# Optimization experiments

Hardware: AMD Instinct MI355X
Metric: run time of the kernel (lower is better)

Reference implementation:

```python
import jax, jax.numpy as jnp
import numpy as np

BS = 2; D = 256; NH = 8; NL = 4; NP = 4; WS = 7; DFF = 1024
SHAPES = [(92, 92), (46, 46), (23, 23), (12, 12)]
LEN = sum(h * w for h, w in SHAPES)  # 11253
DH = D // NH


def _layer_norm(x, g, b):
    mu = jnp.mean(x, -1, keepdims=True)
    var = jnp.var(x, -1, keepdims=True)
    return (x - mu) * jax.lax.rsqrt(var + 1e-5) * g + b


def _bilinear(v_l, loc, H_, W_):
    # v_l: (N, nh, H_*W_, d); loc: (N, Lq, nh, P, 2) normalized in [0,1] (x, y)
    N, Lq, nh, P, _ = loc.shape
    x = loc[..., 0] * W_ - 0.5  # grid_sample align_corners=False convention
    y = loc[..., 1] * H_ - 0.5
    x0f = jnp.floor(x); y0f = jnp.floor(y)
    tx = (x - x0f).transpose(0, 2, 1, 3)  # (N, nh, Lq, P)
    ty = (y - y0f).transpose(0, 2, 1, 3)
    x0 = x0f.astype(jnp.int32).transpose(0, 2, 1, 3)
    y0 = y0f.astype(jnp.int32).transpose(0, 2, 1, 3)

    def g(yi, xi):
        valid = ((xi >= 0) & (xi < W_) & (yi >= 0) & (yi < H_)).astype(v_l.dtype)
        idx = (jnp.clip(yi, 0, H_ - 1) * W_ + jnp.clip(xi, 0, W_ - 1)).reshape(N, nh, Lq * P)
        out = jnp.take_along_axis(v_l, idx[..., None], axis=2).reshape(N, nh, Lq, P, -1)
        return out * valid[..., None]

    return (g(y0, x0) * ((1 - tx) * (1 - ty))[..., None]
            + g(y0, x0 + 1) * (tx * (1 - ty))[..., None]
            + g(y0 + 1, x0) * ((1 - tx) * ty)[..., None]
            + g(y0 + 1, x0 + 1) * (tx * ty)[..., None])


def setup_inputs() -> dict:
    key = jax.random.key(0)
    ks = jax.random.split(key, 20)
    s = 0.02
    inp = {}
    inp['src'] = jax.random.normal(ks[0], (BS, LEN, D), jnp.float32)
    inp['pos'] = jax.random.normal(ks[1], (BS, LEN, D), jnp.float32)
    inp['reference_points'] = jax.random.uniform(ks[2], (BS, LEN, NL, 2), jnp.float32)
    c = WS // 2
    ys, xs = jnp.meshgrid(jnp.arange(WS) - c, jnp.arange(WS) - c, indexing='ij')
    inp['window_grid'] = jnp.stack([xs, ys], -1).reshape(WS * WS, 2).astype(jnp.float32)
    for l, (h, w) in enumerate(SHAPES):
        inp[f'mask{l}'] = jax.random.normal(ks[3 + l], (BS, 1, h, w), jnp.float32)
    inp['spatial_shapes'] = jnp.array(SHAPES, jnp.int32)
    starts = np.cumsum([0] + [h * w for h, w in SHAPES])[:NL]
    inp['level_start_index'] = jnp.array(starts, jnp.int32)
    # parse_mask: Conv2d(1, n_heads, 1) per level -> per-head scale + bias
    inp['pm_w'] = jax.random.normal(ks[7], (NL, NH), jnp.float32) * s
    inp['pm_b'] = jax.random.normal(ks[8], (NL, NH), jnp.float32) * s
    inp['Wv'] = jax.random.normal(ks[9], (D, D), jnp.float32) * s
    inp['bv'] = jnp.zeros((D,), jnp.float32)
    inp['Wo'] = jax.random.normal(ks[10], (D, D), jnp.float32) * s
    inp['bo'] = jnp.zeros((D,), jnp.float32)
    inp['ln1_g'] = jnp.ones((D,), jnp.float32)
    inp['ln1_b'] = jnp.zeros((D,), jnp.float32)
    inp['W1'] = jax.random.normal(ks[11], (D, DFF), jnp.float32) * s
    inp['b1'] = jnp.zeros((DFF,), jnp.float32)
    inp['W2'] = jax.random.normal(ks[12], (DFF, D), jnp.float32) * s
    inp['b2'] = jnp.zeros((D,), jnp.float32)
    inp['ln2_g'] = jnp.ones((D,), jnp.float32)
    inp['ln2_b'] = jnp.zeros((D,), jnp.float32)
    return inp


def reference(src, pos, reference_points, window_grid, mask0, mask1, mask2, mask3,
              spatial_shapes, level_start_index, pm_w, pm_b, Wv, bv, Wo, bo,
              ln1_g, ln1_b, W1, b1, W2, b2, ln2_g, ln2_b):
    masks = [mask0, mask1, mask2, mask3]
    p = WS // 2
    offs, samp = [], []
    for l, (H_, W_) in enumerate(SHAPES):
        # 1x1 conv from 1 -> NH channels
        m = masks[l] * pm_w[l][None, :, None, None] + pm_b[l][None, :, None, None]  # (BS,NH,H,W)
        mp = jnp.pad(m, ((0, 0), (0, 0), (p, p), (p, p)))
        # unfold: (BS, NH, WS*WS, H*W), kernel positions row-major
        patches = jnp.stack([mp[:, :, i:i + H_, j:j + W_] for i in range(WS) for j in range(WS)], axis=2)
        patches = patches.reshape(BS, NH, WS * WS, H_ * W_).transpose(0, 1, 3, 2)  # (BS,NH,HW,WS^2)
        vals, idx = jax.lax.top_k(patches, NP)  # (BS,NH,HW,NP)
        off = window_grid[idx]  # (BS,NH,HW,NP,2)
        offs.append(off.transpose(0, 2, 1, 3, 4))   # (BS,HW,NH,NP,2)
        samp.append(vals.transpose(0, 2, 1, 3))     # (BS,HW,NH,NP)
    offsets = jnp.concatenate(offs, axis=1)       # (BS,LEN,NH,NP,2)
    pred_sampled = jnp.concatenate(samp, axis=1)  # (BS,LEN,NH,NP)

    # MSDeformAttn (encoder mode: external offsets + mask-derived attention logits)
    value = (src @ Wv + bv).reshape(BS, LEN, NH, DH)
    attn = jax.nn.softmax(
        jnp.broadcast_to(pred_sampled[:, :, :, None, :], (BS, LEN, NH, NL, NP)).reshape(BS, LEN, NH, NL * NP),
        axis=-1).reshape(BS, LEN, NH, NL, NP)
    norm = jnp.array([[w, h] for h, w in SHAPES], jnp.float32)  # (NL, 2) as (W, H)
    loc = reference_points[:, :, None, :, None, :] + offsets[:, :, :, None, :, :] / norm[None, None, None, :, None, :]

    out = jnp.zeros((BS, LEN, NH, DH), src.dtype)
    s0 = 0
    for l, (H_, W_) in enumerate(SHAPES):
        v_l = value[:, s0:s0 + H_ * W_].transpose(0, 2, 1, 3)  # (BS,NH,HW,DH)
        sampled = _bilinear(v_l, loc[:, :, :, l], H_, W_)       # (BS,NH,LEN,NP,DH)
        out = out + jnp.einsum('nhqpd,nqhp->nqhd', sampled, attn[:, :, :, l])
        s0 += H_ * W_
    attn_out = out.reshape(BS, LEN, D) @ Wo + bo

    x = _layer_norm(src + attn_out, ln1_g, ln1_b)
    x2 = jax.nn.relu(x @ W1 + b1) @ W2 + b2
    return _layer_norm(x + x2, ln2_g, ln2_b)
```

## Files before the change

kernel.cpp:

```cpp
#include <hip/hip_runtime.h>
#include <cstddef>
#include <cstdint>

#define LEN_T 11253
#define TOK   22506
#define NHEADS 8
#define DMODEL 256

#define SBAR() __builtin_amdgcn_sched_barrier(0)

typedef __attribute__((ext_vector_type(8))) short short8;
typedef __attribute__((ext_vector_type(4))) float f32x4;

__device__ __forceinline__ unsigned short f2bf(float f) {
  union { float f; unsigned u; } v; v.f = f;
  unsigned r = v.u + 0x7fffu + ((v.u >> 16) & 1u);
  return (unsigned short)(r >> 16);
}
__device__ __forceinline__ float bfhi2f(unsigned u) {
  union { unsigned u; float f; } v; v.u = u & 0xffff0000u; return v.f;
}
__device__ __forceinline__ float bflo2f(unsigned u) {
  union { unsigned u; float f; } v; v.u = u << 16; return v.f;
}
__device__ __forceinline__ float bf2f(unsigned short s) {
  union { unsigned u; float f; } v; v.u = (unsigned)s << 16; return v.f;
}
__device__ __forceinline__ void gld_lds16(const void* g, void* l) {
  __builtin_amdgcn_global_load_lds(
      (const __attribute__((address_space(1))) void*)g,
      (__attribute__((address_space(3))) void*)l, 16, 0, 0);
}

__device__ __forceinline__ void ins4(float v, int ji,
    float& t0, float& t1, float& t2, float& t3,
    int& i0, int& i1, int& i2, int& i3)
{
  bool a0 = v > t0, a1 = v > t1, a2 = v > t2, a3 = v > t3;
  t3 = a3 ? (a2 ? t2 : v) : t3;  i3 = a3 ? (a2 ? i2 : ji) : i3;
  t2 = a2 ? (a1 ? t1 : v) : t2;  i2 = a2 ? (a1 ? i1 : ji) : i2;
  t1 = a1 ? (a0 ? t0 : v) : t1;  i1 = a1 ? (a0 ? i0 : ji) : i1;
  t0 = a0 ? v : t0;              i0 = a0 ? ji : i0;
}

__global__ __launch_bounds__(256) void pre_kernel(
    const float* __restrict__ m0, const float* __restrict__ m1,
    const float* __restrict__ m2, const float* __restrict__ m3,
    const float* __restrict__ pm_w, const float* __restrict__ pm_b,
    const float* __restrict__ Wv, const float* __restrict__ Wo,
    const float* __restrict__ W1, const float* __restrict__ W2,
    unsigned short* __restrict__ Wv_g, unsigned short* __restrict__ Wo_g,
    unsigned short* __restrict__ W1_g, unsigned short* __restrict__ W2_g,
    unsigned* __restrict__ offp, float* __restrict__ attw)
{
  int blk = blockIdx.x;
  if (blk >= 704) {
    int cb = blk - 704;
    const float* W; unsigned short* Bg; int lgN, base;
    if (cb < 32)       { W = Wv; Bg = Wv_g; lgN = 8;  base = cb; }
    else if (cb < 64)  { W = Wo; Bg = Wo_g; lgN = 8;  base = cb - 32; }
    else if (cb < 192) { W = W1; Bg = W1_g; lgN = 10; base = cb - 64; }
    else               { W = W2; Bg = W2_g; lgN = 8;  base = cb - 192; }
    int idx = base * 256 + threadIdx.x;
    int s   = idx & 3;
    int n   = (idx >> 2) & ((1 << lgN) - 1);
    int kb  = idx >> (2 + lgN);
    int k0  = kb * 32 + ((s ^ ((n + (n >> 2)) & 3)) << 3);
    const float* wp = W + (size_t)k0 * (1 << lgN) + n;
    unsigned short e[8];
    #pragma unroll
    for (int j = 0; j < 8; ++j) e[j] = f2bf(wp[(size_t)j << lgN]);
    uint4 o;
    o.x = (unsigned)e[0] | ((unsigned)e[1] << 16);
    o.y = (unsigned)e[2] | ((unsigned)e[3] << 16);
    o.z = (unsigned)e[4] | ((unsigned)e[5] << 16);
    o.w = (unsigned)e[6] | ((unsigned)e[7] << 16);
    *(uint4*)(Bg + (size_t)idx * 8) = o;
    return;
  }
  int t = blk * 256 + threadIdx.x;
  if (t >= TOK * NHEADS) return;
  int h  = t & 7;
  int bq = t >> 3;
  int b  = bq / LEN_T;
  int q  = bq - b * LEN_T;
  int l, H_, W_;
  const float* mk;
  if (q < 8464)       { l = 0; H_ = 92; W_ = 92; mk = m0; }
  else if (q < 10580) { l = 1; H_ = 46; W_ = 46; mk = m1; }
  else if (q < 11109) { l = 2; H_ = 23; W_ = 23; mk = m2; }
  else                { l = 3; H_ = 12; W_ = 12; mk = m3; }
  int st = (l == 0) ? 0 : (l == 1) ? 8464 : (l == 2) ? 10580 : 11109;
  int pos = q - st;
  int rr = pos / W_;
  int cc = pos - rr * W_;
  float w  = pm_w[l * NHEADS + h];
  float bb = pm_b[l * NHEADS + h];
  const float* mp = mk + (size_t)b * H_ * W_;

  float t0=-1e30f,t1=-1e30f,t2=-1e30f,t3=-1e30f;
  int   i0=0,i1=0,i2=0,i3=0;
  for (int i = 0; i < 7; ++i) {
    int yy = rr + i - 3;
    #pragma unroll
    for (int j = 0; j < 7; ++j) {
      int xx = cc + j - 3;
      float v = 0.f;
      if (yy >= 0 && yy < H_ && xx >= 0 && xx < W_)
        v = mp[(size_t)yy * W_ + xx] * w + bb;
      ins4(v, j | (i << 4), t0, t1, t2, t3, i0, i1, i2, i3);
    }
  }
  float e1 = __expf(t1 - t0);
  float e2 = __expf(t2 - t0);
  float e3 = __expf(t3 - t0);
  float inv = 1.f / (4.f * (1.f + e1 + e2 + e3));
  float4 wout; wout.x = inv; wout.y = e1 * inv; wout.z = e2 * inv; wout.w = e3 * inv;
  *(float4*)(attw + (size_t)t * 4) = wout;
  offp[t] = (unsigned)i0 | ((unsigned)i1 << 8)
          | ((unsigned)i2 << 16) | ((unsigned)i3 << 24);
}

__global__ __launch_bounds__(256) void sample_kernel(
    const unsigned short* __restrict__ Vb, const float* __restrict__ refpts,
    const unsigned* __restrict__ offp, const float* __restrict__ attw,
    unsigned short* __restrict__ outp)
{
  __shared__ int4  sidx[4][128];
  __shared__ float4 swgt[4][128];
  const int wv   = threadIdx.x >> 6;
  const int lane = threadIdx.x & 63;
  const int bx = blockIdx.x & 7, by = blockIdx.x >> 3;
  const int nb = bx * 703 + min(bx, 3) + by;
  const int blk = nb * 4 + wv;
  const bool ok = blk < TOK;

  if (ok) {
    const int b = (blk >= LEN_T) ? 1 : 0;
    const float* rp = refpts + (size_t)blk * 8;
    #pragma unroll
    for (int e = 0; e < 2; ++e) {
      int t = lane * 2 + e;
      int h = t & 7, lp = t >> 3;
      int l = lp >> 2, p = lp & 3;
      unsigned pb = (offp[(size_t)blk * 8 + h] >> (8 * p)) & 0xffu;
      float ox = (float)(int)(pb & 15u) - 3.f;
      float oy = (float)(int)(pb >> 4)  - 3.f;
      float aw = attw[((size_t)blk * 8 + h) * 4 + p];
      int H_ = (l == 0) ? 92 : (l == 1) ? 46 : (l == 2) ? 23 : 12;
      int st = (l == 0) ? 0  : (l == 1) ? 8464 : (l == 2) ? 10580 : 11109;
      float xx = rp[2 * l]     * (float)H_ - 0.5f + ox;
      float yy = rp[2 * l + 1] * (float)H_ - 0.5f + oy;
      float x0f = floorf(xx), y0f = floorf(yy);
      float tx = xx - x0f, ty = yy - y0f;
      int x0 = (int)x0f, y0 = (int)y0f;
      int base = b * LEN_T + st;
      float wc[4] = {(1.f - tx) * (1.f - ty), tx * (1.f - ty),
                     (1.f - tx) * ty,         tx * ty};
      int4 idx; float4 wg;
      int xs[4] = {x0, x0 + 1, x0, x0 + 1};
      int ys[4] = {y0, y0, y0 + 1, y0 + 1};
      int   id[4]; float wgt[4];
      #pragma unroll
      for (int c = 0; c < 4; ++c) {
        int xi = xs[c], yi = ys[c];
        bool v_ = (xi >= 0) & (xi < H_) & (yi >= 0) & (yi < H_);
        id[c]  = base + min(max(yi, 0), H_ - 1) * H_ + min(max(xi, 0), H_ - 1);
        wgt[c] = v_ ? aw * wc[c] : 0.f;
      }
      idx.x = id[0]; idx.y = id[1]; idx.z = id[2]; idx.w = id[3];
      wg.x = wgt[0]; wg.y = wgt[1]; wg.z = wgt[2]; wg.w = wgt[3];
      sidx[wv][t] = idx;
      swgt[wv][t] = wg;
    }
  }
  __syncthreads();

  if (ok) {
    const int h = lane >> 3, dg = lane & 7;
    const unsigned short* vb = Vb + h * 32 + dg * 4;
    f32x4 acc = {0.f, 0.f, 0.f, 0.f};

    uint2  u[2][8];
    float4 wg[2][2];

    #pragma unroll
    for (int j = 0; j < 2; ++j) {
      int4 idx  = sidx[wv][j * 8 + h];
      wg[0][j]  = swgt[wv][j * 8 + h];
      u[0][j*4+0] = *(const uint2*)(vb + (size_t)idx.x * DMODEL);
      u[0][j*4+1] = *(const uint2*)(vb + (size_t)idx.y * DMODEL);
      u[0][j*4+2] = *(const uint2*)(vb + (size_t)idx.z * DMODEL);
      u[0][j*4+3] = *(const uint2*)(vb + (size_t)idx.w * DMODEL);
    }
    SBAR();
    #pragma unroll
    for (int bt = 0; bt < 8; ++bt) {
      const int cur = bt & 1, nxt = cur ^ 1;
      if (bt < 7) {
        #pragma unroll
        for (int j = 0; j < 2; ++j) {
          int lp = (bt + 1) * 2 + j;
          int4 idx   = sidx[wv][lp * 8 + h];
          wg[nxt][j] = swgt[wv][lp * 8 + h];
          u[nxt][j*4+0] = *(const uint2*)(vb + (size_t)idx.x * DMODEL);
          u[nxt][j*4+1] = *(const uint2*)(vb + (size_t)idx.y * DMODEL);
          u[nxt][j*4+2] = *(const uint2*)(vb + (size_t)idx.z * DMODEL);
          u[nxt][j*4+3] = *(const uint2*)(vb + (size_t)idx.w * DMODEL);
        }
      }
      SBAR();
      #pragma unroll
      for (int j = 0; j < 2; ++j) {
        const float4 w4 = wg[cur][j];
        const uint2 u0 = u[cur][j*4+0], u1 = u[cur][j*4+1];
        const uint2 u2 = u[cur][j*4+2], u3 = u[cur][j*4+3];
        acc.x += w4.x * bflo2f(u0.x) + w4.y * bflo2f(u1.x) + w4.z * bflo2f(u2.x) + w4.w * bflo2f(u3.x);
        acc.y += w4.x * bfhi2f(u0.x) + w4.y * bfhi2f(u1.x) + w4.z * bfhi2f(u2.x) + w4.w * bfhi2f(u3.x);
        acc.z += w4.x * bflo2f(u0.y) + w4.y * bflo2f(u1.y) + w4.z * bflo2f(u2.y) + w4.w * bflo2f(u3.y);
        acc.w += w4.x * bfhi2f(u0.y) + w4.y * bfhi2f(u1.y) + w4.z * bfhi2f(u2.y) + w4.w * bfhi2f(u3.y);
      }
    }
    uint2 o;
    o.x = (unsigned)f2bf(acc.x) | ((unsigned)f2bf(acc.y) << 16);
    o.y = (unsigned)f2bf(acc.z) | ((unsigned)f2bf(acc.w) << 16);
    *(uint2*)(outp + (size_t)blk * DMODEL + h * 32 + dg * 4) = o;
  }
}

template<int EPI, bool AF32, int KC>
__global__ __launch_bounds__(256, 3) void gemm_v7(
    const void* __restrict__ Aptr, const unsigned short* __restrict__ Bg,
    const float* __restrict__ bias, const float* __restrict__ res,
    const unsigned short* __restrict__ resb,
    const float* __restrict__ lng, const float* __restrict__ lnb,
    float* __restrict__ C, unsigned short* __restrict__ Cb,
    int M, int N)
{
  constexpr int K  = KC * 256;
  constexpr int NK = KC * 8;
  __shared__ short As[2][32 * 32]  __attribute__((aligned(16)));
  __shared__ short Bs[2][256 * 32] __attribute__((aligned(16)));
  __shared__ float2 lnred[32][4];
  const int tid = threadIdx.x, w = tid >> 6, lane = tid & 63;
  const int row0  = blockIdx.x * 32;
  const int ncol0 = blockIdx.y * 256;
  const int wn0   = ncol0 + w * 64;
  const int colq = lane & 15, quad = lane >> 4;

  f32x4 acc[2][4];
  #pragma unroll
  for (int i = 0; i < 2; ++i)
    #pragma unroll
    for (int j = 0; j < 4; ++j) acc[i][j] = (f32x4){0.f, 0.f, 0.f, 0.f};

  const int rA   = min(row0 + (tid >> 2), M - 1);
  const int ksw8 = (((tid & 3) ^ ((tid >> 3) & 3)) << 3);
  const float* Af = (const float*)Aptr;
  const short* Ab = (const short*)Aptr;

  auto stageA = [&](int kb, int nbuf) {
    if (tid < 128) {
      if constexpr (AF32) {
        const float* ap = Af + (size_t)rA * K + kb * 32 + ksw8;
        float4 f0 = *(const float4*)ap;
        float4 f1 = *(const float4*)(ap + 4);
        uint4 u;
        u.x = (unsigned)f2bf(f0.x) | ((unsigned)f2bf(f0.y) << 16);
        u.y = (unsigned)f2bf(f0.z) | ((unsigned)f2bf(f0.w) << 16);
        u.z = (unsigned)f2bf(f1.x) | ((unsigned)f2bf(f1.y) << 16);
        u.w = (unsigned)f2bf(f1.z) | ((unsigned)f2bf(f1.w) << 16);
        *(uint4*)(As[nbuf] + (size_t)tid * 8) = u;
      } else {
        gld_lds16(Ab + (size_t)rA * K + kb * 32 + ksw8,
                  As[nbuf] + (size_t)tid * 8);
      }
    }
  };
  auto stageB = [&](int kb, int nbuf) {
    const unsigned short* slab = Bg + ((size_t)kb * N + ncol0) * 32;
    #pragma unroll
    for (int j = 0; j < 4; ++j)
      gld_lds16(slab + j * 2048 + tid * 8, Bs[nbuf] + j * 2048 + (size_t)tid * 8);
  };

  const int rdoA = ((quad ^ ((colq >> 1) & 3)) << 3);

  stageA(0, 0); stageB(0, 0);
  __syncthreads();
  int buf = 0;
  for (int kb = 0; kb < NK; ++kb) {
    if (kb + 1 < NK) { stageA(kb + 1, buf ^ 1); stageB(kb + 1, buf ^ 1); }
    short8 af[2], bf[4];
    #pragma unroll
    for (int mt = 0; mt < 2; ++mt)
      af[mt] = *(const short8*)(As[buf] + (mt * 16 + colq) * 32 + rdoA);
    #pragma unroll
    for (int nt = 0; nt < 4; ++nt) {
      int nl = w * 64 + nt * 16 + colq;
      bf[nt] = *(const short8*)(Bs[buf] + nl * 32
                                + ((quad ^ ((nl + (nl >> 2)) & 3)) << 3));
    }
    #pragma unroll
    for (int mt = 0; mt < 2; ++mt)
      #pragma unroll
      for (int nt = 0; nt < 4; ++nt)
        acc[mt][nt] = __builtin_amdgcn_mfma_f32_16x16x32_bf16(
            af[mt], bf[nt], acc[mt][nt], 0, 0, 0);
    __syncthreads();
    buf ^= 1;
  }

  float bia[4];
  #pragma unroll
  for (int nt = 0; nt < 4; ++nt) bia[nt] = bias[wn0 + nt * 16 + colq];

  if constexpr (EPI == 1 || EPI == 3) {
    #pragma unroll
    for (int mt = 0; mt < 2; ++mt) {
      #pragma unroll
      for (int r = 0; r < 4; ++r) {
        int lrow = mt * 16 + quad * 4 + r;
        int rowc = min(row0 + lrow, M - 1);
        float s = 0.f, sq = 0.f;
        #pragma unroll
        for (int nt = 0; nt < 4; ++nt) {
          float rv;
          if constexpr (EPI == 1)
            rv = res[(size_t)rowc * 256 + wn0 + nt * 16 + colq];
          else
            rv = bf2f(resb[(size_t)rowc * 256 + wn0 + nt * 16 + colq]);
          float f = acc[mt][nt][r] + bia[nt] + rv;
          acc[mt][nt][r] = f;
          s += f; sq += f * f;
        }
        #pragma unroll
        for (int off = 1; off < 16; off <<= 1) {
          s  += __shfl_xor(s,  off, 64);
          sq += __shfl_xor(sq, off, 64);
        }
        if (colq == 0) lnred[lrow][w] = (float2){s, sq};
      }
    }
    __syncthreads();
    #pragma unroll
    for (int mt = 0; mt < 2; ++mt) {
      #pragma unroll
      for (int r = 0; r < 4; ++r) {
        int lrow = mt * 16 + quad * 4 + r;
        int row  = row0 + lrow;
        if (row >= M) continue;
        float2 p0 = lnred[lrow][0], p1 = lnred[lrow][1];
        float2 p2 = lnred[lrow][2], p3 = lnred[lrow][3];
        float mu  = (p0.x + p1.x + p2.x + p3.x) * (1.f / 256.f);
        float var = (p0.y + p1.y + p2.y + p3.y) * (1.f / 256.f) - mu * mu;
        float rs  = rsqrtf(var + 1e-5f);
        #pragma unroll
        for (int nt = 0; nt < 4; ++nt) {
          int col = wn0 + nt * 16 + colq;
          float o = (acc[mt][nt][r] - mu) * rs * lng[col] + lnb[col];
          if constexpr (EPI == 1)
            Cb[(size_t)row * 256 + col] = f2bf(o);
          else
            C[(size_t)row * 256 + col] = o;
        }
      }
    }
  } else {
    #pragma unroll
    for (int mt = 0; mt < 2; ++mt) {
      #pragma unroll
      for (int r = 0; r < 4; ++r) {
        int row = row0 + mt * 16 + quad * 4 + r;
        if (row < M) {
          #pragma unroll
          for (int nt = 0; nt < 4; ++nt) {
            float f = acc[mt][nt][r] + bia[nt];
            if constexpr (EPI == 2) f = fmaxf(f, 0.f);
            Cb[(size_t)row * N + wn0 + nt * 16 + colq] = f2bf(f);
          }
        }
      }
    }
  }
}

extern "C" void kernel_launch(void* const* d_in, const int* in_sizes, int n_in,
                              void* d_out, int out_size, void* d_ws, size_t ws_size,
                              hipStream_t stream)
{
  const float* src    = (const float*)d_in[0];
  const float* refpts = (const float*)d_in[2];
  const float* m0   = (const float*)d_in[4];
  const float* m1   = (const float*)d_in[5];
  const float* m2   = (const float*)d_in[6];
  const float* m3   = (const float*)d_in[7];
  const float* pm_w = (const float*)d_in[10];
  const float* pm_b = (const float*)d_in[11];
  const float* Wv   = (const float*)d_in[12];
  const float* bv   = (const float*)d_in[13];
  const float* Wo   = (const float*)d_in[14];
  const float* bo   = (const float*)d_in[15];
  const float* ln1g = (const float*)d_in[16];
  const float* ln1b = (const float*)d_in[17];
  const float* W1   = (const float*)d_in[18];
  const float* b1   = (const float*)d_in[19];
  const float* W2   = (const float*)d_in[20];
  const float* b2   = (const float*)d_in[21];
  const float* ln2g = (const float*)d_in[22];
  const float* ln2b = (const float*)d_in[23];
  float* out = (float*)d_out;
  char*  w   = (char*)d_ws;

  unsigned short* Vb      = (unsigned short*)(w);
  unsigned short* attnpre = (unsigned short*)(w + 11523072);
  unsigned short* h1      = (unsigned short*)(w + 23046144);
  char*           tail    = w + 69138432;
  float*          attw    = (float*)(tail);
  unsigned*       offp    = (unsigned*)(tail + 2880768);
  unsigned short* Wv_g    = (unsigned short*)(tail + 3600960);
  unsigned short* Wo_g    = (unsigned short*)(tail + 3732032);
  unsigned short* W1_g    = (unsigned short*)(tail + 3863104);
  unsigned short* W2_g    = (unsigned short*)(tail + 4387392);
  unsigned short* x_bf    = attnpre;

  pre_kernel<<<dim3(1024), 256, 0, stream>>>(
      m0, m1, m2, m3, pm_w, pm_b, Wv, Wo, W1, W2,
      Wv_g, Wo_g, W1_g, W2_g, offp, attw);

  gemm_v7<0, true, 1><<<dim3(704, 1), 256, 0, stream>>>(
      src, Wv_g, bv, nullptr, nullptr, nullptr, nullptr,
      nullptr, Vb, TOK, 256);

  sample_kernel<<<dim3(5627), 256, 0, stream>>>(
      Vb, refpts, offp, attw, attnpre);

  gemm_v7<1, false, 1><<<dim3(704, 1), 256, 0, stream>>>(
      attnpre, Wo_g, bo, src, nullptr, ln1g, ln1b,
      nullptr, x_bf, TOK, 256);

  gemm_v7<2, false, 1><<<dim3(704, 4), 256, 0, stream>>>(
      x_bf, W1_g, b1, nullptr, nullptr, nullptr, nullptr,
      nullptr, h1, TOK, 1024);

  gemm_v7<3, false, 4><<<dim3(704, 1), 256, 0, stream>>>(
      h1, W2_g, b2, nullptr, x_bf, ln2g, ln2b,
      out, nullptr, TOK, 256);
}
```

Baseline: 272.7 us.

## Stage full 256-wide K chunks into LDS per GEMM block instead of double-buffering

```diff
diff --git a/kernel.cpp b/kernel.cpp
--- a/kernel.cpp
+++ b/kernel.cpp
@@ -65,7 +65,7 @@
     int s   = idx & 3;
     int n   = (idx >> 2) & ((1 << lgN) - 1);
     int kb  = idx >> (2 + lgN);
-    int k0  = kb * 32 + ((s ^ ((n + (n >> 2)) & 3)) << 3);
+    int k0  = kb * 32 + ((s ^ ((n >> 1) & 3)) << 3);
     const float* wp = W + (size_t)k0 * (1 << lgN) + n;
     unsigned short e[8];
     #pragma unroll
@@ -229,7 +229,7 @@
 }
 
 template<int EPI, bool AF32, int KC>
-__global__ __launch_bounds__(256, 3) void gemm_v7(
+__global__ __launch_bounds__(256, 1) void gemm_v8(
     const void* __restrict__ Aptr, const unsigned short* __restrict__ Bg,
     const float* __restrict__ bias, const float* __restrict__ res,
     const unsigned short* __restrict__ resb,
@@ -237,10 +237,9 @@
     float* __restrict__ C, unsigned short* __restrict__ Cb,
     int M, int N)
 {
-  constexpr int K  = KC * 256;
-  constexpr int NK = KC * 8;
-  __shared__ short As[2][32 * 32]  __attribute__((aligned(16)));
-  __shared__ short Bs[2][256 * 32] __attribute__((aligned(16)));
+  constexpr int K = KC * 256;
+  __shared__ short As[32 * 256]   __attribute__((aligned(16)));
+  __shared__ short Bs[8][256 * 32] __attribute__((aligned(16)));
   __shared__ float2 lnred[32][4];
   const int tid = threadIdx.x, w = tid >> 6, lane = tid & 63;
   const int row0  = blockIdx.x * 32;
@@ -254,15 +253,22 @@
     #pragma unroll
     for (int j = 0; j < 4; ++j) acc[i][j] = (f32x4){0.f, 0.f, 0.f, 0.f};
 
-  const int rA   = min(row0 + (tid >> 2), M - 1);
-  const int ksw8 = (((tid & 3) ^ ((tid >> 3) & 3)) << 3);
   const float* Af = (const float*)Aptr;
   const short* Ab = (const short*)Aptr;
-
-  auto stageA = [&](int kb, int nbuf) {
-    if (tid < 128) {
+  const int rdo = ((quad ^ ((colq >> 1) & 3)) << 3);
+
+  for (int c = 0; c < KC; ++c) {
+    if (c > 0) __syncthreads();
+    #pragma unroll
+    for (int j = 0; j < 4; ++j) {
+      const int o  = j * 2048 + tid * 8;
+      const int r  = o >> 8;
+      const int kb = (o >> 5) & 7;
+      const int s  = (o >> 3) & 3;
+      const int gk = c * 256 + kb * 32 + ((s ^ ((r >> 1) & 3)) << 3);
+      const int rA = min(row0 + r, M - 1);
       if constexpr (AF32) {
-        const float* ap = Af + (size_t)rA * K + kb * 32 + ksw8;
+        const float* ap = Af + (size_t)rA * K + gk;
         float4 f0 = *(const float4*)ap;
         float4 f1 = *(const float4*)(ap + 4);
         uint4 u;
@@ -270,45 +276,38 @@
         u.y = (unsigned)f2bf(f0.z) | ((unsigned)f2bf(f0.w) << 16);
         u.z = (unsigned)f2bf(f1.x) | ((unsigned)f2bf(f1.y) << 16);
         u.w = (unsigned)f2bf(f1.z) | ((unsigned)f2bf(f1.w) << 16);
-        *(uint4*)(As[nbuf] + (size_t)tid * 8) = u;
+        *(uint4*)(As + o) = u;
       } else {
-        gld_lds16(Ab + (size_t)rA * K + kb * 32 + ksw8,
-                  As[nbuf] + (size_t)tid * 8);
-      }
-    }
-  };
-  auto stageB = [&](int kb, int nbuf) {
-    const unsigned short* slab = Bg + ((size_t)kb * N + ncol0) * 32;
-    #pragma unroll
-    for (int j = 0; j < 4; ++j)
-      gld_lds16(slab + j * 2048 + tid * 8, Bs[nbuf] + j * 2048 + (size_t)tid * 8);
-  };
-
-  const int rdoA = ((quad ^ ((colq >> 1) & 3)) << 3);
-
-  stageA(0, 0); stageB(0, 0);
-  __syncthreads();
-  int buf = 0;
-  for (int kb = 0; kb < NK; ++kb) {
-    if (kb + 1 < NK) { stageA(kb + 1, buf ^ 1); stageB(kb + 1, buf ^ 1); }
-    short8 af[2], bf[4];
-    #pragma unroll
-    for (int mt = 0; mt < 2; ++mt)
-      af[mt] = *(const short8*)(As[buf] + (mt * 16 + colq) * 32 + rdoA);
-    #pragma unroll
-    for (int nt = 0; nt < 4; ++nt) {
-      int nl = w * 64 + nt * 16 + colq;
-      bf[nt] = *(const short8*)(Bs[buf] + nl * 32
-                                + ((quad ^ ((nl + (nl >> 2)) & 3)) << 3));
-    }
-    #pragma unroll
-    for (int mt = 0; mt < 2; ++mt)
+        gld_lds16(Ab + (size_t)rA * K + gk, As + o);
+      }
+    }
+    #pragma unroll
+    for (int kb = 0; kb < 8; ++kb) {
+      const unsigned short* slab = Bg + ((size_t)(c * 8 + kb) * N + ncol0) * 32;
+      #pragma unroll
+      for (int j = 0; j < 4; ++j) {
+        const int o = j * 2048 + tid * 8;
+        gld_lds16(slab + o, &Bs[kb][0] + o);
+      }
+    }
+    __syncthreads();
+    #pragma unroll
+    for (int kb = 0; kb < 8; ++kb) {
+      short8 af[2], bf[4];
+      #pragma unroll
+      for (int mt = 0; mt < 2; ++mt)
+        af[mt] = *(const short8*)(As + (mt * 16 + colq) * 256 + kb * 32 + rdo);
       #pragma unroll
       for (int nt = 0; nt < 4; ++nt)
-        acc[mt][nt] = __builtin_amdgcn_mfma_f32_16x16x32_bf16(
-            af[mt], bf[nt], acc[mt][nt], 0, 0, 0);
-    __syncthreads();
-    buf ^= 1;
+        bf[nt] = *(const short8*)(&Bs[kb][0] + (w * 64 + nt * 16 + colq) * 32
+                                  + rdo);
+      #pragma unroll
+      for (int mt = 0; mt < 2; ++mt)
+        #pragma unroll
+        for (int nt = 0; nt < 4; ++nt)
+          acc[mt][nt] = __builtin_amdgcn_mfma_f32_16x16x32_bf16(
+              af[mt], bf[nt], acc[mt][nt], 0, 0, 0);
+    }
   }
 
   float bia[4];
@@ -428,22 +427,22 @@
       m0, m1, m2, m3, pm_w, pm_b, Wv, Wo, W1, W2,
       Wv_g, Wo_g, W1_g, W2_g, offp, attw);
 
-  gemm_v7<0, true, 1><<<dim3(704, 1), 256, 0, stream>>>(
+  gemm_v8<0, true, 1><<<dim3(704, 1), 256, 0, stream>>>(
       src, Wv_g, bv, nullptr, nullptr, nullptr, nullptr,
       nullptr, Vb, TOK, 256);
 
   sample_kernel<<<dim3(5627), 256, 0, stream>>>(
       Vb, refpts, offp, attw, attnpre);
 
-  gemm_v7<1, false, 1><<<dim3(704, 1), 256, 0, stream>>>(
+  gemm_v8<1, false, 1><<<dim3(704, 1), 256, 0, stream>>>(
       attnpre, Wo_g, bo, src, nullptr, ln1g, ln1b,
       nullptr, x_bf, TOK, 256);
 
-  gemm_v7<2, false, 1><<<dim3(704, 4), 256, 0, stream>>>(
+  gemm_v8<2, false, 1><<<dim3(704, 4), 256, 0, stream>>>(
       x_bf, W1_g, b1, nullptr, nullptr, nullptr, nullptr,
       nullptr, h1, TOK, 1024);
 
-  gemm_v7<3, false, 4><<<dim3(704, 1), 256, 0, stream>>>(
+  gemm_v8<3, false, 4><<<dim3(704, 1), 256, 0, stream>>>(
       h1, W2_g, b2, nullptr, x_bf, ln2g, ln2b,
       out, nullptr, TOK, 256);
 }
```

Measured after the change: 318.4 us. 1.17x slower.

## Fuse FFN up/down GEMMs and LayerNorm into one kernel keeping hidden in LDS

Applied to the files above, without the earlier changes.

```diff
diff --git a/kernel.cpp b/kernel.cpp
--- a/kernel.cpp
+++ b/kernel.cpp
@@ -8,6 +8,9 @@
 #define DMODEL 256
 
 #define SBAR() __builtin_amdgcn_sched_barrier(0)
+#define WVM0() asm volatile("s_waitcnt vmcnt(0)" ::: "memory")
+#define WVM4() asm volatile("s_waitcnt vmcnt(4)" ::: "memory")
+#define WVM8() asm volatile("s_waitcnt vmcnt(8)" ::: "memory")
 
 typedef __attribute__((ext_vector_type(8))) short short8;
 typedef __attribute__((ext_vector_type(4))) float f32x4;
@@ -380,6 +383,179 @@
             Cb[(size_t)row * N + wn0 + nt * 16 + colq] = f2bf(f);
           }
         }
+      }
+    }
+  }
+}
+
+__global__ __launch_bounds__(256, 1) void ffn_kernel(
+    const unsigned short* __restrict__ xb,
+    const unsigned short* __restrict__ W1g,
+    const unsigned short* __restrict__ W2g,
+    const float* __restrict__ b1, const float* __restrict__ b2,
+    const float* __restrict__ lng, const float* __restrict__ lnb,
+    float* __restrict__ out, int M)
+{
+  __shared__ short xs[8 * 1024]    __attribute__((aligned(16)));
+  __shared__ short hs[32 * 1024]   __attribute__((aligned(16)));
+  __shared__ short ws[4][3][2048]  __attribute__((aligned(16)));
+  __shared__ float2 lnred[32][4];
+  const int tid = threadIdx.x, w = tid >> 6, lane = tid & 63;
+  const int row0 = blockIdx.x * 32;
+  const int colq = lane & 15, quad = lane >> 4;
+
+  auto issue = [&](int s) {
+    const unsigned short* src;
+    if (s < 32)
+      src = W1g + ((size_t)((s & 7) * 1024 + w * 256 + (s >> 3) * 64)) * 32;
+    else
+      src = W2g + ((size_t)((s - 32) * 256 + w * 64)) * 32;
+    short* dst = &ws[w][s % 3][0];
+    #pragma unroll
+    for (int j = 0; j < 4; ++j)
+      gld_lds16(src + j * 512 + lane * 8, dst + j * 512 + lane * 8);
+  };
+
+  const int rA   = min(row0 + (tid >> 2), M - 1);
+  const int ksw8 = (((tid & 3) ^ ((tid >> 3) & 3)) << 3);
+  if (tid < 128) {
+    #pragma unroll
+    for (int kb = 0; kb < 8; ++kb)
+      gld_lds16(xb + (size_t)rA * 256 + kb * 32 + ksw8,
+                xs + kb * 1024 + (size_t)tid * 8);
+  }
+  issue(0);
+  issue(1);
+  __syncthreads();
+
+  const int rdoA = ((quad ^ ((colq >> 1) & 3)) << 3);
+  int rdoB[4];
+  #pragma unroll
+  for (int nt = 0; nt < 4; ++nt) {
+    int loc = nt * 16 + colq;
+    rdoB[nt] = ((quad ^ ((loc + (loc >> 2)) & 3)) << 3);
+  }
+
+  f32x4 acc[2][4];
+  for (int g = 0; g < 4; ++g) {
+    #pragma unroll
+    for (int i = 0; i < 2; ++i)
+      #pragma unroll
+      for (int j = 0; j < 4; ++j) acc[i][j] = (f32x4){0.f, 0.f, 0.f, 0.f};
+    float bia1[4];
+    #pragma unroll
+    for (int nt = 0; nt < 4; ++nt) bia1[nt] = b1[w * 256 + g * 64 + nt * 16 + colq];
+
+    #pragma unroll
+    for (int kb = 0; kb < 8; ++kb) {
+      const int s = g * 8 + kb;
+      issue(s + 2);
+      WVM8();
+      const short* cw = &ws[w][s % 3][0];
+      short8 af[2], bf[4];
+      #pragma unroll
+      for (int mt = 0; mt < 2; ++mt)
+        af[mt] = *(const short8*)(xs + kb * 1024 + (mt * 16 + colq) * 32 + rdoA);
+      #pragma unroll
+      for (int nt = 0; nt < 4; ++nt)
+        bf[nt] = *(const short8*)(cw + (nt * 16 + colq) * 32 + rdoB[nt]);
+      #pragma unroll
+      for (int mt = 0; mt < 2; ++mt)
+        #pragma unroll
+        for (int nt = 0; nt < 4; ++nt)
+          acc[mt][nt] = __builtin_amdgcn_mfma_f32_16x16x32_bf16(
+              af[mt], bf[nt], acc[mt][nt], 0, 0, 0);
+    }
+    #pragma unroll
+    for (int mt = 0; mt < 2; ++mt)
+      #pragma unroll
+      for (int nt = 0; nt < 4; ++nt) {
+        const int col = w * 256 + g * 64 + nt * 16 + colq;
+        const int kbh = col >> 5, inc = col & 31;
+        const int sw  = inc >> 3,  e  = inc & 7;
+        #pragma unroll
+        for (int r = 0; r < 4; ++r) {
+          const int row_l = mt * 16 + quad * 4 + r;
+          const int sp = sw ^ ((row_l >> 1) & 3);
+          float f = acc[mt][nt][r] + bia1[nt];
+          f = fmaxf(f, 0.f);
+          hs[kbh * 1024 + row_l * 32 + sp * 8 + e] = (short)f2bf(f);
+        }
+      }
+  }
+  __syncthreads();
+
+  #pragma unroll
+  for (int i = 0; i < 2; ++i)
+    #pragma unroll
+    for (int j = 0; j < 4; ++j) acc[i][j] = (f32x4){0.f, 0.f, 0.f, 0.f};
+  const int wn0 = w * 64;
+
+  for (int k2 = 0; k2 < 32; ++k2) {
+    const int s = 32 + k2;
+    if (s + 2 < 64) issue(s + 2);
+    if (s < 62)      { WVM8(); }
+    else if (s == 62){ WVM4(); }
+    else             { WVM0(); }
+    const short* cw = &ws[w][s % 3][0];
+    short8 af[2], bf[4];
+    #pragma unroll
+    for (int mt = 0; mt < 2; ++mt)
+      af[mt] = *(const short8*)(hs + k2 * 1024 + (mt * 16 + colq) * 32 + rdoA);
+    #pragma unroll
+    for (int nt = 0; nt < 4; ++nt)
+      bf[nt] = *(const short8*)(cw + (nt * 16 + colq) * 32 + rdoB[nt]);
+    #pragma unroll
+    for (int mt = 0; mt < 2; ++mt)
+      #pragma unroll
+      for (int nt = 0; nt < 4; ++nt)
+        acc[mt][nt] = __builtin_amdgcn_mfma_f32_16x16x32_bf16(
+            af[mt], bf[nt], acc[mt][nt], 0, 0, 0);
+  }
+
+  float bia[4];
+  #pragma unroll
+  for (int nt = 0; nt < 4; ++nt) bia[nt] = b2[wn0 + nt * 16 + colq];
+
+  #pragma unroll
+  for (int mt = 0; mt < 2; ++mt) {
+    #pragma unroll
+    for (int r = 0; r < 4; ++r) {
+      int lrow = mt * 16 + quad * 4 + r;
+      int rowc = min(row0 + lrow, M - 1);
+      float s = 0.f, sq = 0.f;
+      #pragma unroll
+      for (int nt = 0; nt < 4; ++nt) {
+        float rv = bf2f(xb[(size_t)rowc * 256 + wn0 + nt * 16 + colq]);
+        float f = acc[mt][nt][r] + bia[nt] + rv;
+        acc[mt][nt][r] = f;
+        s += f; sq += f * f;
+      }
+      #pragma unroll
+      for (int off = 1; off < 16; off <<= 1) {
+        s  += __shfl_xor(s,  off, 64);
+        sq += __shfl_xor(sq, off, 64);
+      }
+      if (colq == 0) lnred[lrow][w] = (float2){s, sq};
+    }
+  }
+  __syncthreads();
+  #pragma unroll
+  for (int mt = 0; mt < 2; ++mt) {
+    #pragma unroll
+    for (int r = 0; r < 4; ++r) {
+      int lrow = mt * 16 + quad * 4 + r;
+      int row  = row0 + lrow;
+      if (row >= M) continue;
+      float2 p0 = lnred[lrow][0], p1 = lnred[lrow][1];
+      float2 p2 = lnred[lrow][2], p3 = lnred[lrow][3];
+      float mu  = (p0.x + p1.x + p2.x + p3.x) * (1.f / 256.f);
+      float var = (p0.y + p1.y + p2.y + p3.y) * (1.f / 256.f) - mu * mu;
+      float rs  = rsqrtf(var + 1e-5f);
+      #pragma unroll
+      for (int nt = 0; nt < 4; ++nt) {
+        int col = wn0 + nt * 16 + colq;
+        out[(size_t)row * 256 + col] = (acc[mt][nt][r] - mu) * rs * lng[col] + lnb[col];
       }
     }
   }
@@ -414,7 +590,6 @@
 
   unsigned short* Vb      = (unsigned short*)(w);
   unsigned short* attnpre = (unsigned short*)(w + 11523072);
-  unsigned short* h1      = (unsigned short*)(w + 23046144);
   char*           tail    = w + 69138432;
   float*          attw    = (float*)(tail);
   unsigned*       offp    = (unsigned*)(tail + 2880768);
@@ -439,11 +614,6 @@
       attnpre, Wo_g, bo, src, nullptr, ln1g, ln1b,
       nullptr, x_bf, TOK, 256);
 
-  gemm_v7<2, false, 1><<<dim3(704, 4), 256, 0, stream>>>(
-      x_bf, W1_g, b1, nullptr, nullptr, nullptr, nullptr,
-      nullptr, h1, TOK, 1024);
-
-  gemm_v7<3, false, 4><<<dim3(704, 1), 256, 0, stream>>>(
-      h1, W2_g, b2, nullptr, x_bf, ln2g, ln2b,
-      out, nullptr, TOK, 256);
-}
+  ffn_kernel<<<dim3(704), 256, 0, stream>>>(
+      x_bf, W1_g, W2_g, b1, b2, ln2g, ln2b, out, TOK);
+}
```

Result: slower. 300.7 us (+10.2%).
